# Kernel optimization log

Hardware: AMD Instinct MI355X
Metric: run time of the kernel (lower is better)

Reference implementation:

```python
import jax, jax.numpy as jnp
import numpy as np

NEW_SEQ_LEN = 150  # hard-coded in the original forward


def _interp_one(x, length):
    """PyTorch F.interpolate(mode='linear', align_corners=False) on x[:length].
    x: [T, D] float, length: scalar int. Returns [NEW_SEQ_LEN, D]."""
    lf = length.astype(jnp.float32)
    scale = lf / NEW_SEQ_LEN
    src = (jnp.arange(NEW_SEQ_LEN, dtype=jnp.float32) + 0.5) * scale - 0.5
    src = jnp.maximum(src, 0.0)
    i0 = jnp.floor(src).astype(jnp.int32)
    i0 = jnp.minimum(i0, length - 1)
    i1 = jnp.minimum(i0 + 1, length - 1)
    w = (src - i0.astype(jnp.float32))[:, None]  # [150, 1]
    return x[i0] * (1.0 - w) + x[i1] * w


_interp_batch = jax.vmap(_interp_one)  # ragged per-sample interpolation, fused over batch


def setup_inputs() -> dict:
    key = jax.random.key(0)
    ks = jax.random.split(key, 8)
    B, T, C_IMU, C_EMG, EMB, CSD = 2048, 512, 48, 16, 64, 256
    x_imu = jax.random.normal(ks[0], (B, T, C_IMU), jnp.float32)
    x_emg = jax.random.normal(ks[1], (B, T, C_EMG), jnp.float32)
    lens = jax.random.randint(ks[2], (B,), 160, T + 1, jnp.int32)  # >= NEW_SEQ_LEN
    w_emb_imu = jax.random.normal(ks[3], (C_IMU, EMB), jnp.float32) / np.sqrt(C_IMU)
    b_emb_imu = jnp.zeros((EMB,), jnp.float32)
    w_emb_emg = jax.random.normal(ks[4], (C_EMG, EMB), jnp.float32) / np.sqrt(C_EMG)
    b_emb_emg = jnp.zeros((EMB,), jnp.float32)
    w_proj = jax.random.normal(ks[5], (NEW_SEQ_LEN * EMB, CSD), jnp.float32) / np.sqrt(NEW_SEQ_LEN * EMB)
    b_proj = jnp.zeros((CSD,), jnp.float32)
    return {"x_imu": x_imu, "x_emg": x_emg, "lens": lens,
            "w_emb_imu": w_emb_imu, "b_emb_imu": b_emb_imu,
            "w_emb_emg": w_emb_emg, "b_emb_emg": b_emb_emg,
            "w_proj": w_proj, "b_proj": b_proj}


def reference(x_imu, x_emg, lens, w_emb_imu, b_emb_imu, w_emb_emg, b_emb_emg, w_proj, b_proj):
    B = x_imu.shape[0]
    # embedding nets (per-timestep linear encoders) -> [B, T, 64]
    seq_imu = jnp.einsum('btc,ce->bte', x_imu, w_emb_imu) + b_emb_imu
    seq_emg = jnp.einsum('btc,ce->bte', x_emg, w_emb_emg) + b_emb_emg
    # ragged linear interpolation of each sample's first lens[i] steps to 150
    seq_imu = _interp_batch(seq_imu, lens)  # [B, 150, 64]
    seq_emg = _interp_batch(seq_emg, lens)
    # flatten and project; NOTE: original code applies linear_proj_imu to BOTH
    out_imu = seq_imu.reshape(B, -1) @ w_proj + b_proj
    out_emg = seq_emg.reshape(B, -1) @ w_proj + b_proj
    return (out_imu, out_emg)
```

## Files before the change

### kernel.cpp

```cpp
#include <hip/hip_runtime.h>

#define NEWL 150
#define EMBD 64
#define NCOL 256
#define CIMU 48
#define CEMG 16

#define KIMU (NEWL * CIMU)
#define KEMG (NEWL * CEMG)
#define KSTI 225
#define KSTE 75
#define NCI 4
#define NCE 2

typedef __bf16 bf16x8_t __attribute__((ext_vector_type(8)));
typedef __bf16 bf16x4_t __attribute__((ext_vector_type(4)));
typedef float f32x4_t __attribute__((ext_vector_type(4)));

__device__ __forceinline__ f32x4_t mfma16(bf16x8_t a, bf16x8_t b, f32x4_t c) {
  return __builtin_amdgcn_mfma_f32_16x16x32_bf16(a, b, c, 0, 0, 0);
}

template <int C, int KST>
__device__ void wcomb_body(const float* __restrict__ wemb,
                           const float* __restrict__ wreg_src,
                           __bf16* __restrict__ wpk, int s, int j) {
  float wreg[EMBD];
#pragma unroll
  for (int e = 0; e < EMBD; ++e) wreg[e] = wreg_src[(size_t)e * NCOL];
  const int cb = j >> 4, lr = j & 15;
#pragma unroll
  for (int q = 0; q < C / 8; ++q) {
    const int kq = (s * C) / 8 + q;
    const int ks = kq >> 2, h = kq & 3;
    bf16x8_t tv;
#pragma unroll
    for (int u = 0; u < 8; ++u) {
      const float* we = wemb + (q * 8 + u) * EMBD;
      float acc = 0.f;
#pragma unroll
      for (int e = 0; e < EMBD; ++e) acc = fmaf(we[e], wreg[e], acc);
      tv[u] = (__bf16)acc;
    }
    *(bf16x8_t*)(wpk + (((size_t)cb * KST + ks) * 64 + h * 16 + lr) * 8) = tv;
  }
}

__global__ __launch_bounds__(256) void wcomb_kernel(
    const float* __restrict__ w_emb_imu, const float* __restrict__ w_emb_emg,
    const float* __restrict__ b_emb_imu, const float* __restrict__ b_emb_emg,
    const float* __restrict__ w_proj,
    __bf16* __restrict__ wpk_imu, __bf16* __restrict__ wpk_emg,
    float* __restrict__ bpart) {
  const int s = blockIdx.x;
  const int m = blockIdx.y;
  const int j = threadIdx.x;
  const float* wp_base = w_proj + (size_t)s * EMBD * NCOL + j;
  const float* be = (m == 0) ? b_emb_imu : b_emb_emg;
  float bacc = 0.f;
#pragma unroll
  for (int e = 0; e < EMBD; ++e) bacc = fmaf(be[e], wp_base[(size_t)e * NCOL], bacc);
  bpart[((size_t)m * NEWL + s) * NCOL + j] = bacc;
  if (m == 0)
    wcomb_body<CIMU, KSTI>(w_emb_imu, wp_base, wpk_imu, s, j);
  else
    wcomb_body<CEMG, KSTE>(w_emb_emg, wp_base, wpk_emg, s, j);
}

__global__ __launch_bounds__(256, 4) void fused_kernel(
    const float* __restrict__ x_imu, const float* __restrict__ x_emg,
    const int* __restrict__ lens,
    const __bf16* __restrict__ wpk_imu, const __bf16* __restrict__ wpk_emg,
    const float* __restrict__ b_proj, const float* __restrict__ bpart,
    float* __restrict__ p_imu, float* __restrict__ p_emg,
    float* __restrict__ bias, int B, int T) {
  const int bid = blockIdx.x;
  const int span = B >> 4;
  const int nblk = (NCE + NCI) * span;
  if (bid == nblk) {
    const int j = threadIdx.x;
#pragma unroll
    for (int m = 0; m < 2; ++m) {
      float acc = b_proj[j];
      for (int s = 0; s < NEWL; ++s) acc += bpart[((size_t)m * NEWL + s) * NCOL + j];
      bias[m * NCOL + j] = acc;
    }
    return;
  }

  __shared__ __bf16 lds[2][2][3][512];

  const int tid = threadIdx.x;
  const int wv = tid >> 6, l = tid & 63;

  const int rank = (bid & 7) * (nblk >> 3) + (bid >> 3);
  const int cs = rank / span;
  const int r2 = rank - cs * span;
  const int mt = r2 >> 1;
  const int nh = r2 & 1;
  const bool is_imu = cs >= NCE;
  const int c = is_imu ? cs - NCE : cs;

  int g0, NG;
  if (is_imu) { g0 = 19 * c; NG = (c < 3) ? 19 : 18; }
  else        { g0 = 13 * c; NG = c ? 12 : 13; }
  const int ks0 = 3 * g0;
  const int sb = is_imu ? 2 * g0 : 6 * g0;

  const __bf16* Wp = is_imu ? wpk_imu : wpk_emg;
  const int KST = is_imu ? KSTI : KSTE;
  float* P = is_imu ? (p_imu + (size_t)c * B * NCOL) : (p_emg + (size_t)c * B * NCOL);

  const size_t PS = (size_t)KST * 512;
  const __bf16* bg = Wp + ((size_t)(nh * 8 + wv * 2) * KST + ks0) * 512 + l * 8;

  const int q = tid & 3, sl = (tid >> 2) & 1, bli = tid >> 3;
  const int ble = tid / 6, se = tid - ble * 6;
  const bool act = is_imu || (tid < 192);
  const int b_g = mt * 32 + (is_imu ? bli : (act ? ble : 0));
  int lenv = 1;
  float scale = 0.f;
  if (act) { lenv = lens[b_g]; scale = (float)lenv * (1.0f / 150.0f); }

  float gr[32];
  float wS;
  bf16x8_t bB[6];
  f32x4_t acc00 = {0.f, 0.f, 0.f, 0.f}, acc01 = acc00, acc10 = acc00, acc11 = acc00;

#define ISSUE_GI(g2) do {                                                       \
    const int s_ = sb + (g2) * 2 + sl;                                          \
    float src_ = fmaxf(((float)s_ + 0.5f) * scale - 0.5f, 0.0f);                \
    int i0_ = min((int)src_, lenv - 1);                                         \
    int i1_ = min(i0_ + 1, lenv - 1);                                           \
    wS = src_ - (float)i0_;                                                     \
    const float* r0_ = x_imu + ((size_t)b_g * T + i0_) * CIMU + q * 4;          \
    const float* r1_ = x_imu + ((size_t)b_g * T + i1_) * CIMU + q * 4;          \
    _Pragma("unroll")                                                           \
    for (int t = 0; t < 3; ++t) {                                               \
      float4 v_ = *(const float4*)(r0_ + t * 16);                               \
      gr[t * 4 + 0] = v_.x; gr[t * 4 + 1] = v_.y;                               \
      gr[t * 4 + 2] = v_.z; gr[t * 4 + 3] = v_.w;                               \
      float4 u_ = *(const float4*)(r1_ + t * 16);                               \
      gr[12 + t * 4 + 0] = u_.x; gr[12 + t * 4 + 1] = u_.y;                     \
      gr[12 + t * 4 + 2] = u_.z; gr[12 + t * 4 + 3] = u_.w;                     \
    }                                                                           \
  } while (0)

#define LERP_WI(BUF) do {                                                       \
    const float wg_ = wS, om_ = 1.0f - wg_;                                     \
    _Pragma("unroll")                                                           \
    for (int t = 0; t < 3; ++t) {                                               \
      bf16x4_t o_;                                                              \
      _Pragma("unroll")                                                         \
      for (int u = 0; u < 4; ++u)                                               \
        o_[u] = (__bf16)(gr[t * 4 + u] * om_ + gr[12 + t * 4 + u] * wg_);       \
      const int kq_ = sl * 6 + t * 2 + (q >> 1);                                \
      *(bf16x4_t*)(&lds[BUF][bli >> 4][kq_ >> 2]                                \
                       [((kq_ & 3) * 16 + (bli & 15)) * 8 + (q & 1) * 4]) = o_; \
    }                                                                           \
  } while (0)

#define ISSUE_GE(g2) do { if (act) {                                            \
    const int s_ = sb + (g2) * 6 + se;                                          \
    float src_ = fmaxf(((float)s_ + 0.5f) * scale - 0.5f, 0.0f);                \
    int i0_ = min((int)src_, lenv - 1);                                         \
    int i1_ = min(i0_ + 1, lenv - 1);                                           \
    wS = src_ - (float)i0_;                                                     \
    const float* p0_ = x_emg + ((size_t)b_g * T + i0_) * CEMG;                  \
    const float* p1_ = x_emg + ((size_t)b_g * T + i1_) * CEMG;                  \
    _Pragma("unroll")                                                           \
    for (int t = 0; t < 4; ++t) {                                               \
      float4 v_ = *(const float4*)(p0_ + t * 4);                                \
      gr[t * 4 + 0] = v_.x; gr[t * 4 + 1] = v_.y;                               \
      gr[t * 4 + 2] = v_.z; gr[t * 4 + 3] = v_.w;                               \
      float4 u_ = *(const float4*)(p1_ + t * 4);                                \
      gr[16 + t * 4 + 0] = u_.x; gr[16 + t * 4 + 1] = u_.y;                     \
      gr[16 + t * 4 + 2] = u_.z; gr[16 + t * 4 + 3] = u_.w;                     \
    }                                                                           \
  } } while (0)

#define LERP_WE(BUF) do { if (act) {                                            \
    const float wg_ = wS, om_ = 1.0f - wg_;                                     \
    _Pragma("unroll")                                                           \
    for (int t2 = 0; t2 < 2; ++t2) {                                            \
      bf16x8_t o_;                                                              \
      _Pragma("unroll")                                                         \
      for (int u = 0; u < 8; ++u)                                               \
        o_[u] = (__bf16)(gr[t2 * 8 + u] * om_ + gr[16 + t2 * 8 + u] * wg_);     \
      const int kq_ = se * 2 + t2;                                              \
      *(bf16x8_t*)(&lds[BUF][ble >> 4][kq_ >> 2]                                \
                       [((kq_ & 3) * 16 + (ble & 15)) * 8]) = o_;               \
    }                                                                           \
  } } while (0)

#define ISSUE_B(g1) do {                                                        \
    const __bf16* pb_ = bg + (size_t)((g1) * 3) * 512;                          \
    _Pragma("unroll")                                                           \
    for (int ks = 0; ks < 3; ++ks) {                                            \
      bB[ks * 2 + 0] = *(const bf16x8_t*)(pb_ + (size_t)ks * 512);              \
      bB[ks * 2 + 1] = *(const bf16x8_t*)(pb_ + PS + (size_t)ks * 512);         \
    }                                                                           \
  } while (0)

#define COMPUTE(Pp) do {                                                        \
    _Pragma("unroll")                                                           \
    for (int ks = 0; ks < 3; ++ks) {                                            \
      bf16x8_t a0_ = *(const bf16x8_t*)(&lds[Pp][0][ks][l * 8]);                \
      bf16x8_t a1_ = *(const bf16x8_t*)(&lds[Pp][1][ks][l * 8]);                \
      acc00 = mfma16(a0_, bB[ks * 2 + 0], acc00);                               \
      acc01 = mfma16(a0_, bB[ks * 2 + 1], acc01);                               \
      acc10 = mfma16(a1_, bB[ks * 2 + 0], acc10);                               \
      acc11 = mfma16(a1_, bB[ks * 2 + 1], acc11);                               \
    }                                                                           \
  } while (0)

  if (is_imu) { ISSUE_GI(0); LERP_WI(0); }
  else        { ISSUE_GE(0); LERP_WE(0); }
  ISSUE_B(0);
  __syncthreads();

  for (int p = 0; p < NG; ++p) {
    const int more = (p + 1 < NG);
    if (more) { if (is_imu) ISSUE_GI(p + 1); else ISSUE_GE(p + 1); }
    COMPUTE(p & 1);
    if (more) ISSUE_B(p + 1);
    if (more) { if (is_imu) LERP_WI((p + 1) & 1); else LERP_WE((p + 1) & 1); }
    __syncthreads();
  }

  const int lh = l >> 4, lr = l & 15;
  float* Pb = P + (size_t)(mt * 32 + lh * 4) * NCOL + nh * 128 + wv * 32 + lr;
#pragma unroll
  for (int jj = 0; jj < 4; ++jj) {
    Pb[(size_t)jj * NCOL] = acc00[jj];
    Pb[(size_t)jj * NCOL + 16] = acc01[jj];
    Pb[(size_t)(16 + jj) * NCOL] = acc10[jj];
    Pb[(size_t)(16 + jj) * NCOL + 16] = acc11[jj];
  }
#undef ISSUE_GI
#undef LERP_WI
#undef ISSUE_GE
#undef LERP_WE
#undef ISSUE_B
#undef COMPUTE
}

__global__ __launch_bounds__(256) void combine_kernel(
    const float* __restrict__ bias, const float* __restrict__ p_imu,
    const float* __restrict__ p_emg, float* __restrict__ out, int B) {
  const int b = blockIdx.x, m = blockIdx.y, j = threadIdx.x;
  const size_t n = (size_t)B * NCOL;
  const size_t o = (size_t)b * NCOL + j;
  if (m == 0) {
    float v = bias[j];
#pragma unroll
    for (int c = 0; c < NCI; ++c) v += p_imu[c * n + o];
    out[o] = v;
  } else {
    out[n + o] = bias[NCOL + j] + p_emg[o] + p_emg[n + o];
  }
}

extern "C" void kernel_launch(void* const* d_in, const int* in_sizes, int n_in,
                              void* d_out, int out_size, void* d_ws, size_t ws_size,
                              hipStream_t stream) {
  const float* x_imu     = (const float*)d_in[0];
  const float* x_emg     = (const float*)d_in[1];
  const int*   lens      = (const int*)d_in[2];
  const float* w_emb_imu = (const float*)d_in[3];
  const float* b_emb_imu = (const float*)d_in[4];
  const float* w_emb_emg = (const float*)d_in[5];
  const float* b_emb_emg = (const float*)d_in[6];
  const float* w_proj    = (const float*)d_in[7];
  const float* b_proj    = (const float*)d_in[8];
  float* out = (float*)d_out;

  const int B = in_sizes[2];
  const int T = in_sizes[0] / (B * CIMU);

  char* ws = (char*)d_ws;
  __bf16* wpk_imu = (__bf16*)ws;  ws += (size_t)NCOL * KIMU * 2;
  __bf16* wpk_emg = (__bf16*)ws;  ws += (size_t)NCOL * KEMG * 2;
  float*  bias    = (float*)ws;   ws += 2 * NCOL * 4;
  float*  bpart   = (float*)ws;   ws += (size_t)2 * NEWL * NCOL * 4;
  float*  p_imu   = (float*)ws;   ws += (size_t)NCI * B * NCOL * 4;
  float*  p_emg   = (float*)ws;   ws += (size_t)NCE * B * NCOL * 4;

  wcomb_kernel<<<dim3(NEWL, 2), 256, 0, stream>>>(
      w_emb_imu, w_emb_emg, b_emb_imu, b_emb_emg, w_proj, wpk_imu, wpk_emg, bpart);
  const int span = B >> 4;
  const int nblk = (NCE + NCI) * span + 1;
  fused_kernel<<<nblk, 256, 0, stream>>>(x_imu, x_emg, lens, wpk_imu, wpk_emg,
                                         b_proj, bpart, p_imu, p_emg, bias, B, T);
  combine_kernel<<<dim3(B, 2), 256, 0, stream>>>(bias, p_imu, p_emg, out, B);
}
```

Before: 82.86 us.

## Use 512-thread blocks covering all 256 columns and split gather rows across lane pairs

```diff
diff --git a/kernel.cpp b/kernel.cpp
--- a/kernel.cpp
+++ b/kernel.cpp
@@ -67,7 +67,7 @@
     wcomb_body<CEMG, KSTE>(w_emb_emg, wp_base, wpk_emg, s, j);
 }
 
-__global__ __launch_bounds__(256, 4) void fused_kernel(
+__global__ __launch_bounds__(512, 2) void fused_kernel(
     const float* __restrict__ x_imu, const float* __restrict__ x_emg,
     const int* __restrict__ lens,
     const __bf16* __restrict__ wpk_imu, const __bf16* __restrict__ wpk_emg,
@@ -75,15 +75,18 @@
     float* __restrict__ p_imu, float* __restrict__ p_emg,
     float* __restrict__ bias, int B, int T) {
   const int bid = blockIdx.x;
-  const int span = B >> 4;
+  const int span = B >> 5;
   const int nblk = (NCE + NCI) * span;
   if (bid == nblk) {
     const int j = threadIdx.x;
-#pragma unroll
-    for (int m = 0; m < 2; ++m) {
-      float acc = b_proj[j];
-      for (int s = 0; s < NEWL; ++s) acc += bpart[((size_t)m * NEWL + s) * NCOL + j];
-      bias[m * NCOL + j] = acc;
+    if (j < NCOL) {
+#pragma unroll
+      for (int m = 0; m < 2; ++m) {
+        float acc = b_proj[j];
+        for (int s = 0; s < NEWL; ++s)
+          acc += bpart[((size_t)m * NEWL + s) * NCOL + j];
+        bias[m * NCOL + j] = acc;
+      }
     }
     return;
   }
@@ -93,11 +96,8 @@
   const int tid = threadIdx.x;
   const int wv = tid >> 6, l = tid & 63;
 
-  const int rank = (bid & 7) * (nblk >> 3) + (bid >> 3);
-  const int cs = rank / span;
-  const int r2 = rank - cs * span;
-  const int mt = r2 >> 1;
-  const int nh = r2 & 1;
+  const int cs = bid / span;
+  const int mt = bid - cs * span;
   const bool is_imu = cs >= NCE;
   const int c = is_imu ? cs - NCE : cs;
 
@@ -112,17 +112,19 @@
   float* P = is_imu ? (p_imu + (size_t)c * B * NCOL) : (p_emg + (size_t)c * B * NCOL);
 
   const size_t PS = (size_t)KST * 512;
-  const __bf16* bg = Wp + ((size_t)(nh * 8 + wv * 2) * KST + ks0) * 512 + l * 8;
-
-  const int q = tid & 3, sl = (tid >> 2) & 1, bli = tid >> 3;
-  const int ble = tid / 6, se = tid - ble * 6;
-  const bool act = is_imu || (tid < 192);
-  const int b_g = mt * 32 + (is_imu ? bli : (act ? ble : 0));
+  const __bf16* bg = Wp + ((size_t)(wv * 2) * KST + ks0) * 512 + l * 8;
+
+  const int q = tid & 3, rowb = (tid >> 2) & 1;
+  const int pid = tid >> 3, b4 = pid & 31, sl = pid >> 5;
+  const int pid_e = tid >> 1;
+  const int ble = pid_e / 6, se = pid_e - ble * 6, rowe = tid & 1;
+  const bool act = is_imu || (tid < 384);
+  const int b_g = mt * 32 + (is_imu ? b4 : (act ? ble : 0));
   int lenv = 1;
   float scale = 0.f;
   if (act) { lenv = lens[b_g]; scale = (float)lenv * (1.0f / 150.0f); }
 
-  float gr[32];
+  float gr[16];
   float wS;
   bf16x8_t bB[6];
   f32x4_t acc00 = {0.f, 0.f, 0.f, 0.f}, acc01 = acc00, acc10 = acc00, acc11 = acc00;
@@ -133,16 +135,13 @@
     int i0_ = min((int)src_, lenv - 1);                                         \
     int i1_ = min(i0_ + 1, lenv - 1);                                           \
     wS = src_ - (float)i0_;                                                     \
-    const float* r0_ = x_imu + ((size_t)b_g * T + i0_) * CIMU + q * 4;          \
-    const float* r1_ = x_imu + ((size_t)b_g * T + i1_) * CIMU + q * 4;          \
+    const float* r_ =                                                           \
+        x_imu + ((size_t)b_g * T + (rowb ? i1_ : i0_)) * CIMU + q * 4;          \
     _Pragma("unroll")                                                           \
     for (int t = 0; t < 3; ++t) {                                               \
-      float4 v_ = *(const float4*)(r0_ + t * 16);                               \
+      float4 v_ = *(const float4*)(r_ + t * 16);                                \
       gr[t * 4 + 0] = v_.x; gr[t * 4 + 1] = v_.y;                               \
       gr[t * 4 + 2] = v_.z; gr[t * 4 + 3] = v_.w;                               \
-      float4 u_ = *(const float4*)(r1_ + t * 16);                               \
-      gr[12 + t * 4 + 0] = u_.x; gr[12 + t * 4 + 1] = u_.y;                     \
-      gr[12 + t * 4 + 2] = u_.z; gr[12 + t * 4 + 3] = u_.w;                     \
     }                                                                           \
   } while (0)
 
@@ -150,13 +149,20 @@
     const float wg_ = wS, om_ = 1.0f - wg_;                                     \
     _Pragma("unroll")                                                           \
     for (int t = 0; t < 3; ++t) {                                               \
-      bf16x4_t o_;                                                              \
-      _Pragma("unroll")                                                         \
-      for (int u = 0; u < 4; ++u)                                               \
-        o_[u] = (__bf16)(gr[t * 4 + u] * om_ + gr[12 + t * 4 + u] * wg_);       \
-      const int kq_ = sl * 6 + t * 2 + (q >> 1);                                \
-      *(bf16x4_t*)(&lds[BUF][bli >> 4][kq_ >> 2]                                \
-                       [((kq_ & 3) * 16 + (bli & 15)) * 8 + (q & 1) * 4]) = o_; \
+      float p0_ = __shfl_xor(gr[t * 4 + 0], 4);                                 \
+      float p1_ = __shfl_xor(gr[t * 4 + 1], 4);                                 \
+      float p2_ = __shfl_xor(gr[t * 4 + 2], 4);                                 \
+      float p3_ = __shfl_xor(gr[t * 4 + 3], 4);                                 \
+      if (rowb == 0) {                                                          \
+        bf16x4_t o_;                                                            \
+        o_[0] = (__bf16)(gr[t * 4 + 0] * om_ + p0_ * wg_);                      \
+        o_[1] = (__bf16)(gr[t * 4 + 1] * om_ + p1_ * wg_);                      \
+        o_[2] = (__bf16)(gr[t * 4 + 2] * om_ + p2_ * wg_);                      \
+        o_[3] = (__bf16)(gr[t * 4 + 3] * om_ + p3_ * wg_);                      \
+        const int kq_ = sl * 6 + t * 2 + (q >> 1);                              \
+        *(bf16x4_t*)(&lds[BUF][b4 >> 4][kq_ >> 2]                               \
+                         [((kq_ & 3) * 16 + (b4 & 15)) * 8 + (q & 1) * 4]) = o_;\
+      }                                                                         \
     }                                                                           \
   } while (0)
 
@@ -166,16 +172,12 @@
     int i0_ = min((int)src_, lenv - 1);                                         \
     int i1_ = min(i0_ + 1, lenv - 1);                                           \
     wS = src_ - (float)i0_;                                                     \
-    const float* p0_ = x_emg + ((size_t)b_g * T + i0_) * CEMG;                  \
-    const float* p1_ = x_emg + ((size_t)b_g * T + i1_) * CEMG;                  \
+    const float* r_ = x_emg + ((size_t)b_g * T + (rowe ? i1_ : i0_)) * CEMG;    \
     _Pragma("unroll")                                                           \
     for (int t = 0; t < 4; ++t) {                                               \
-      float4 v_ = *(const float4*)(p0_ + t * 4);                                \
+      float4 v_ = *(const float4*)(r_ + t * 4);                                 \
       gr[t * 4 + 0] = v_.x; gr[t * 4 + 1] = v_.y;                               \
       gr[t * 4 + 2] = v_.z; gr[t * 4 + 3] = v_.w;                               \
-      float4 u_ = *(const float4*)(p1_ + t * 4);                                \
-      gr[16 + t * 4 + 0] = u_.x; gr[16 + t * 4 + 1] = u_.y;                     \
-      gr[16 + t * 4 + 2] = u_.z; gr[16 + t * 4 + 3] = u_.w;                     \
     }                                                                           \
   } } while (0)
 
@@ -183,13 +185,18 @@
     const float wg_ = wS, om_ = 1.0f - wg_;                                     \
     _Pragma("unroll")                                                           \
     for (int t2 = 0; t2 < 2; ++t2) {                                            \
-      bf16x8_t o_;                                                              \
+      float pv_[8];                                                             \
       _Pragma("unroll")                                                         \
-      for (int u = 0; u < 8; ++u)                                               \
-        o_[u] = (__bf16)(gr[t2 * 8 + u] * om_ + gr[16 + t2 * 8 + u] * wg_);     \
-      const int kq_ = se * 2 + t2;                                              \
-      *(bf16x8_t*)(&lds[BUF][ble >> 4][kq_ >> 2]                                \
-                       [((kq_ & 3) * 16 + (ble & 15)) * 8]) = o_;               \
+      for (int u = 0; u < 8; ++u) pv_[u] = __shfl_xor(gr[t2 * 8 + u], 1);       \
+      if (rowe == 0) {                                                          \
+        bf16x8_t o_;                                                            \
+        _Pragma("unroll")                                                       \
+        for (int u = 0; u < 8; ++u)                                             \
+          o_[u] = (__bf16)(gr[t2 * 8 + u] * om_ + pv_[u] * wg_);                \
+        const int kq_ = se * 2 + t2;                                            \
+        *(bf16x8_t*)(&lds[BUF][ble >> 4][kq_ >> 2]                              \
+                         [((kq_ & 3) * 16 + (ble & 15)) * 8]) = o_;             \
+      }                                                                         \
     }                                                                           \
   } } while (0)
 
@@ -229,7 +236,7 @@
   }
 
   const int lh = l >> 4, lr = l & 15;
-  float* Pb = P + (size_t)(mt * 32 + lh * 4) * NCOL + nh * 128 + wv * 32 + lr;
+  float* Pb = P + (size_t)(mt * 32 + lh * 4) * NCOL + wv * 32 + lr;
 #pragma unroll
   for (int jj = 0; jj < 4; ++jj) {
     Pb[(size_t)jj * NCOL] = acc00[jj];
@@ -288,9 +295,9 @@
 
   wcomb_kernel<<<dim3(NEWL, 2), 256, 0, stream>>>(
       w_emb_imu, w_emb_emg, b_emb_imu, b_emb_emg, w_proj, wpk_imu, wpk_emg, bpart);
-  const int span = B >> 4;
+  const int span = B >> 5;
   const int nblk = (NCE + NCI) * span + 1;
-  fused_kernel<<<nblk, 256, 0, stream>>>(x_imu, x_emg, lens, wpk_imu, wpk_emg,
+  fused_kernel<<<nblk, 512, 0, stream>>>(x_imu, x_emg, lens, wpk_imu, wpk_emg,
                                          b_proj, bpart, p_imu, p_emg, bias, B, T);
   combine_kernel<<<dim3(B, 2), 256, 0, stream>>>(bias, p_imu, p_emg, out, B);
 }
```

Result: faster. 81.03 us (-2.2%).
